# Kernel tuning notes

Measured on AMD Instinct MI355X. Metric: run time of the kernel, lower is better.

Reference implementation:

```python
import jax, jax.numpy as jnp
import numpy as np

D = 6
EPS = 1e-5


def layer_norm(x, w, b):
    m = jnp.mean(x, axis=-1, keepdims=True)
    v = jnp.mean(jnp.square(x - m), axis=-1, keepdims=True)
    return (x - m) * jax.lax.rsqrt(v + EPS) * w + b


def setup_inputs() -> dict:
    key = jax.random.key(0)
    ks = jax.random.split(key, 8)
    B, S = 8192, 128
    scale = 0.2
    return {
        "x": jax.random.normal(ks[0], (B, S, D), jnp.float32),
        "ln1_w": jnp.ones((D,), jnp.float32),
        "ln1_b": jnp.zeros((D,), jnp.float32),
        "wqkv": jax.random.normal(ks[1], (D, 3 * D), jnp.float32) * scale,
        "bqkv": jnp.zeros((3 * D,), jnp.float32),
        "wo": jax.random.normal(ks[2], (D, D), jnp.float32) * scale,
        "bo": jnp.zeros((D,), jnp.float32),
        "ln2_w": jnp.ones((D,), jnp.float32),
        "ln2_b": jnp.zeros((D,), jnp.float32),
        "w1": jax.random.normal(ks[3], (D, D), jnp.float32) * scale,
        "b1": jnp.zeros((D,), jnp.float32),
        "w2": jax.random.normal(ks[4], (D, D), jnp.float32) * scale,
        "b2": jnp.zeros((D,), jnp.float32),
    }


def reference(x, ln1_w, ln1_b, wqkv, bqkv, wo, bo, ln2_w, ln2_b, w1, b1, w2, b2):
    B, S, _ = x.shape
    # --- attention sub-block: x = x + attn(ln1(x)) ---
    h = layer_norm(x, ln1_w, ln1_b)                      # [B,S,D]
    qkv = h @ wqkv + bqkv                                # [B,S,3D]
    q, k, v = jnp.split(qkv, 3, axis=-1)
    scores = jnp.einsum('bqd,bkd->bqk', q, k) / jnp.sqrt(jnp.asarray(D, x.dtype))
    causal = jnp.tril(jnp.ones((S, S), bool))            # [S,S]
    scores = jnp.where(causal, scores, jnp.asarray(-1e9, x.dtype))
    attn = jax.nn.softmax(scores, axis=-1)               # [B,S,S]
    o = jnp.einsum('bqk,bkd->bqd', attn, v) @ wo + bo
    x = x + o
    # --- FFN sub-block: x = x + W2 @ gelu(W1 @ ln2(x)) ---
    h2 = layer_norm(x, ln2_w, ln2_b)
    ff = jax.nn.gelu(h2 @ w1 + b1, approximate=False) @ w2 + b2
    return x + ff
```

## Files before the change

kernel.cpp:

```cpp
#include <hip/hip_runtime.h>
#include <cmath>


typedef float    v2f  __attribute__((ext_vector_type(2)));
typedef float    f4v  __attribute__((ext_vector_type(4)));
typedef short    s4v  __attribute__((ext_vector_type(4)));
typedef uint32_t u2   __attribute__((ext_vector_type(2)));

constexpr int D = 6;
constexpr int S = 128;
#define EPS 1e-5f
#define RSQRT_D 0.4082482904638631f
#define LOG2E   1.4426950408889634f

#define EXP2F(x) __builtin_amdgcn_exp2f(x)
#define RCPF(x)  __builtin_amdgcn_rcpf(x)
#define PKFMA(a, b, c) __builtin_elementwise_fma((a), (b), (c))

union UA { uint32_t u[2]; u2 h; s4v v; };

__device__ __forceinline__ uint32_t pkbf(float hi, float lo) {
    return __builtin_amdgcn_perm(__builtin_bit_cast(uint32_t, hi),
                                 __builtin_bit_cast(uint32_t, lo),
                                 0x07060302u);
}
__device__ __forceinline__ uint16_t bf16t(float x) {
    return (uint16_t)(__builtin_bit_cast(uint32_t, x) >> 16);
}

__device__ __forceinline__ f4v mfma16(s4v a, s4v b, f4v c) {
#if __has_builtin(__builtin_amdgcn_mfma_f32_16x16x16bf16_1k)
    return __builtin_amdgcn_mfma_f32_16x16x16bf16_1k(a, b, c, 0, 0, 0);
#else
    f4v d;
    asm volatile("v_mfma_f32_16x16x16_bf16 %0, %1, %2, %3\n\t"
                 "s_nop 7\n\ts_nop 2"
                 : "=v"(d) : "v"(a), "v"(b), "v"(c));
    return d;
#endif
}

template<int QA, int QB>
__device__ __forceinline__ void attn_pair(
    const UA (&kf)[8], const UA (&vf)[8],
    UA qfA, UA qfB, float (*obuf)[10], int l15, int lq)
{
    const f4v z = {0.f, 0.f, 0.f, 0.f};
    f4v OA0 = z, OA1 = z, OB0 = z, OB1 = z;
    #pragma unroll
    for (int jt = 0; jt <= QB; ++jt) {
        f4v cB = mfma16(kf[jt].v, qfB.v, z);
        f4v cA;
        if (jt <= QA) cA = mfma16(kf[jt].v, qfA.v, z);
        float pB0 = EXP2F(cB[0]);
        float pB1 = EXP2F(cB[1]);
        float pB2 = EXP2F(cB[2]);
        float pB3 = EXP2F(cB[3]);
        if (jt == QB) {
            pB0 = (lq * 4 + 0 > l15) ? 0.f : pB0;
            pB1 = (lq * 4 + 1 > l15) ? 0.f : pB1;
            pB2 = (lq * 4 + 2 > l15) ? 0.f : pB2;
            pB3 = (lq * 4 + 3 > l15) ? 0.f : pB3;
        }
        UA paB;
        paB.u[0] = pkbf(pB1, pB0);
        paB.u[1] = pkbf(pB3, pB2);
        if (jt & 1) OB1 = mfma16(paB.v, vf[jt].v, OB1);
        else        OB0 = mfma16(paB.v, vf[jt].v, OB0);
        if (jt <= QA) {
            float pA0 = EXP2F(cA[0]);
            float pA1 = EXP2F(cA[1]);
            float pA2 = EXP2F(cA[2]);
            float pA3 = EXP2F(cA[3]);
            if (jt == QA) {
                pA0 = (lq * 4 + 0 > l15) ? 0.f : pA0;
                pA1 = (lq * 4 + 1 > l15) ? 0.f : pA1;
                pA2 = (lq * 4 + 2 > l15) ? 0.f : pA2;
                pA3 = (lq * 4 + 3 > l15) ? 0.f : pA3;
            }
            UA paA;
            paA.u[0] = pkbf(pA1, pA0);
            paA.u[1] = pkbf(pA3, pA2);
            if (jt & 1) OA1 = mfma16(paA.v, vf[jt].v, OA1);
            else        OA0 = mfma16(paA.v, vf[jt].v, OA0);
        }
    }
    f4v OA = OA0 + OA1;
    f4v OB = OB0 + OB1;
    if (l15 < 7) {
        #pragma unroll
        for (int r = 0; r < 4; ++r) {
            obuf[QA * 16 + lq * 4 + r][l15] = OA[r];
            obuf[QB * 16 + lq * 4 + r][l15] = OB[r];
        }
    }
}

__global__ __launch_bounds__(S, 4) void txblock_kernel(
    const float* __restrict__ x,
    const float* __restrict__ ln1_w, const float* __restrict__ ln1_b,
    const float* __restrict__ wqkv,  const float* __restrict__ bqkv,
    const float* __restrict__ wo,    const float* __restrict__ bo,
    const float* __restrict__ ln2_w, const float* __restrict__ ln2_b,
    const float* __restrict__ w1,    const float* __restrict__ b1,
    const float* __restrict__ w2,    const float* __restrict__ b2,
    float* __restrict__ out)
{
    __shared__ uint32_t qlds[S][6];
    __shared__ uint32_t klds[S][6];
    __shared__ uint16_t vt[8][S + 8];
    __shared__ float    obuf[S][10];

    const int b = blockIdx.x;
    const int s = threadIdx.x;
    const float* xrow = x + ((size_t)b * S + s) * D;
    float*      orow = out + ((size_t)b * S + s) * D;

    v2f xv01 = ((const v2f*)xrow)[0];
    v2f xv23 = ((const v2f*)xrow)[1];
    v2f xv45 = ((const v2f*)xrow)[2];
    float xv[D] = {xv01[0], xv01[1], xv23[0], xv23[1], xv45[0], xv45[1]};

    float m = 0.f;
    #pragma unroll
    for (int d = 0; d < D; ++d) m += xv[d];
    m *= (1.0f / D);
    float var = 0.f;
    #pragma unroll
    for (int d = 0; d < D; ++d) { float t = xv[d] - m; var += t * t; }
    var *= (1.0f / D);
    float rstd = rsqrtf(var + EPS);
    float h1[D];
    #pragma unroll
    for (int d = 0; d < D; ++d)
        h1[d] = (xv[d] - m) * rstd * ln1_w[d] + ln1_b[d];

    v2f aq[3], ak[3], av[3];
    #pragma unroll
    for (int jp = 0; jp < 3; ++jp) {
        aq[jp] = ((const v2f*)bqkv)[jp];
        ak[jp] = ((const v2f*)(bqkv + D))[jp];
        av[jp] = ((const v2f*)(bqkv + 2 * D))[jp];
    }
    #pragma unroll
    for (int d = 0; d < D; ++d) {
        const float* wrow = wqkv + d * 3 * D;
        v2f hd = {h1[d], h1[d]};
        #pragma unroll
        for (int jp = 0; jp < 3; ++jp) {
            aq[jp] = PKFMA(hd, ((const v2f*)wrow)[jp], aq[jp]);
            ak[jp] = PKFMA(hd, ((const v2f*)(wrow + D))[jp], ak[jp]);
            av[jp] = PKFMA(hd, ((const v2f*)(wrow + 2 * D))[jp], av[jp]);
        }
    }
    const v2f qscale = {RSQRT_D * LOG2E, RSQRT_D * LOG2E};

    #pragma unroll
    for (int jp = 0; jp < 3; ++jp) {
        v2f qs = aq[jp] * qscale;
        qlds[s][jp] = pkbf(qs[1], qs[0]);
        klds[s][jp] = pkbf(ak[jp][1], ak[jp][0]);
    }
    qlds[s][3] = 0; qlds[s][4] = 0; qlds[s][5] = 0;
    klds[s][3] = 0; klds[s][4] = 0; klds[s][5] = 0;
    vt[0][s] = bf16t(av[0][0]);
    vt[1][s] = bf16t(av[0][1]);
    vt[2][s] = bf16t(av[1][0]);
    vt[3][s] = bf16t(av[1][1]);
    vt[4][s] = bf16t(av[2][0]);
    vt[5][s] = bf16t(av[2][1]);
    vt[6][s] = 0x3F80;
    vt[7][s] = 0;
    __syncthreads();

    const int wv  = s >> 6;
    const int l15 = s & 15;
    const int lq  = (s >> 4) & 3;
    const int aoff = (lq < 2) ? lq * 8 : 16;
    const int vne  = (l15 < 7) ? l15 : 7;

    UA kf[8], vf[8];
    #pragma unroll
    for (int jt = 0; jt < 8; ++jt) {
        kf[jt].h = *(const u2*)((const char*)&klds[jt * 16 + l15][0] + aoff);
        vf[jt].h = *(const u2*)&vt[vne][jt * 16 + lq * 4];
    }

    if (wv == 0) {
        UA qA1, qB1, qA2, qB2;
        qA1.h = *(const u2*)((const char*)&qlds[0 * 16 + l15][0] + aoff);
        qB1.h = *(const u2*)((const char*)&qlds[7 * 16 + l15][0] + aoff);
        qA2.h = *(const u2*)((const char*)&qlds[3 * 16 + l15][0] + aoff);
        qB2.h = *(const u2*)((const char*)&qlds[4 * 16 + l15][0] + aoff);
        attn_pair<0, 7>(kf, vf, qA1, qB1, obuf, l15, lq);
        attn_pair<3, 4>(kf, vf, qA2, qB2, obuf, l15, lq);
    } else {
        UA qA1, qB1, qA2, qB2;
        qA1.h = *(const u2*)((const char*)&qlds[1 * 16 + l15][0] + aoff);
        qB1.h = *(const u2*)((const char*)&qlds[6 * 16 + l15][0] + aoff);
        qA2.h = *(const u2*)((const char*)&qlds[2 * 16 + l15][0] + aoff);
        qB2.h = *(const u2*)((const char*)&qlds[5 * 16 + l15][0] + aoff);
        attn_pair<1, 6>(kf, vf, qA1, qB1, obuf, l15, lq);
        attn_pair<2, 5>(kf, vf, qA2, qB2, obuf, l15, lq);
    }
    __syncthreads();

    v2f o01 = *(const v2f*)&obuf[s][0];
    v2f o23 = *(const v2f*)&obuf[s][2];
    v2f o45 = *(const v2f*)&obuf[s][4];
    float invl = RCPF(obuf[s][6]);
    v2f il = {invl, invl};
    o01 *= il; o23 *= il; o45 *= il;
    float av6[D] = {o01[0], o01[1], o23[0], o23[1], o45[0], o45[1]};

    v2f xvp[3] = {xv01, xv23, xv45};
    v2f x2p[3];
    #pragma unroll
    for (int dp = 0; dp < 3; ++dp) {
        v2f o = ((const v2f*)bo)[dp];
        #pragma unroll
        for (int e = 0; e < D; ++e) {
            v2f we = ((const v2f*)(wo + e * D))[dp];
            v2f ae = {av6[e], av6[e]};
            o = PKFMA(ae, we, o);
        }
        x2p[dp] = o + xvp[dp];
    }
    float x2[D] = {x2p[0][0], x2p[0][1], x2p[1][0], x2p[1][1], x2p[2][0], x2p[2][1]};

    float m2 = 0.f;
    #pragma unroll
    for (int d = 0; d < D; ++d) m2 += x2[d];
    m2 *= (1.0f / D);
    float var2 = 0.f;
    #pragma unroll
    for (int d = 0; d < D; ++d) { float t = x2[d] - m2; var2 += t * t; }
    var2 *= (1.0f / D);
    float rstd2 = rsqrtf(var2 + EPS);
    float h2[D];
    #pragma unroll
    for (int d = 0; d < D; ++d)
        h2[d] = (x2[d] - m2) * rstd2 * ln2_w[d] + ln2_b[d];

    v2f ap[3];
    #pragma unroll
    for (int jp = 0; jp < 3; ++jp) {
        v2f a = ((const v2f*)b1)[jp];
        #pragma unroll
        for (int d = 0; d < D; ++d) {
            v2f wd = ((const v2f*)(w1 + d * D))[jp];
            v2f hd = {h2[d], h2[d]};
            a = PKFMA(hd, wd, a);
        }
        ap[jp] = a;
    }
    float g[D];
    #pragma unroll
    for (int j = 0; j < D; ++j) {
        float a = ap[j >> 1][j & 1];
        float t  = a * a;
        float in = fmaf(0.044715f * t, a, a);
        float e  = EXP2F(in * -2.3022229f);
        float r  = RCPF(1.0f + e);
        g[j] = a * r;
    }
    #pragma unroll
    for (int dp = 0; dp < 3; ++dp) {
        v2f a = ((const v2f*)b2)[dp];
        #pragma unroll
        for (int e = 0; e < D; ++e) {
            v2f we = ((const v2f*)(w2 + e * D))[dp];
            v2f ge = {g[e], g[e]};
            a = PKFMA(ge, we, a);
        }
        ((v2f*)orow)[dp] = x2p[dp] + a;
    }
}

extern "C" void kernel_launch(void* const* d_in, const int* in_sizes, int n_in,
                              void* d_out, int out_size, void* d_ws, size_t ws_size,
                              hipStream_t stream) {
    const float* x     = (const float*)d_in[0];
    const float* ln1_w = (const float*)d_in[1];
    const float* ln1_b = (const float*)d_in[2];
    const float* wqkv  = (const float*)d_in[3];
    const float* bqkv  = (const float*)d_in[4];
    const float* wo    = (const float*)d_in[5];
    const float* bo    = (const float*)d_in[6];
    const float* ln2_w = (const float*)d_in[7];
    const float* ln2_b = (const float*)d_in[8];
    const float* w1    = (const float*)d_in[9];
    const float* b1    = (const float*)d_in[10];
    const float* w2    = (const float*)d_in[11];
    const float* b2    = (const float*)d_in[12];
    float* out = (float*)d_out;

    const int B = in_sizes[0] / (S * D);
    txblock_kernel<<<B, S, 0, stream>>>(x, ln1_w, ln1_b, wqkv, bqkv, wo, bo,
                                        ln2_w, ln2_b, w1, b1, w2, b2, out);
}
```

Before: 113.5 us.

## Process multiple batches per block with x prefetch and wave-local epilogue

Each block now loops over four batch elements, prefetching the next batch's input rows into registers while the current one is processed. The input row is stashed in shared memory so each wave can run the output projection and FFN on exactly the rows it produced in attention, removing the barrier between attention and epilogue. The split MFMA accumulators are merged into one chain. This reduces launch/block overhead and hides load latency, at the cost of fewer blocks and a longer dependent MFMA chain.

```diff
diff --git a/kernel.cpp b/kernel.cpp
--- a/kernel.cpp
+++ b/kernel.cpp
@@ -9,6 +9,7 @@
 
 constexpr int D = 6;
 constexpr int S = 128;
+constexpr int NB = 4;
 #define EPS 1e-5f
 #define RSQRT_D 0.4082482904638631f
 #define LOG2E   1.4426950408889634f
@@ -43,10 +44,10 @@
 template<int QA, int QB>
 __device__ __forceinline__ void attn_pair(
     const UA (&kf)[8], const UA (&vf)[8],
-    UA qfA, UA qfB, float (*obuf)[10], int l15, int lq)
+    UA qfA, UA qfB, float (*obuf)[14], int l15, int lq)
 {
     const f4v z = {0.f, 0.f, 0.f, 0.f};
-    f4v OA0 = z, OA1 = z, OB0 = z, OB1 = z;
+    f4v OA = z, OB = z;
     #pragma unroll
     for (int jt = 0; jt <= QB; ++jt) {
         f4v cB = mfma16(kf[jt].v, qfB.v, z);
@@ -65,8 +66,7 @@
         UA paB;
         paB.u[0] = pkbf(pB1, pB0);
         paB.u[1] = pkbf(pB3, pB2);
-        if (jt & 1) OB1 = mfma16(paB.v, vf[jt].v, OB1);
-        else        OB0 = mfma16(paB.v, vf[jt].v, OB0);
+        OB = mfma16(paB.v, vf[jt].v, OB);
         if (jt <= QA) {
             float pA0 = EXP2F(cA[0]);
             float pA1 = EXP2F(cA[1]);
@@ -81,12 +81,9 @@
             UA paA;
             paA.u[0] = pkbf(pA1, pA0);
             paA.u[1] = pkbf(pA3, pA2);
-            if (jt & 1) OA1 = mfma16(paA.v, vf[jt].v, OA1);
-            else        OA0 = mfma16(paA.v, vf[jt].v, OA0);
+            OA = mfma16(paA.v, vf[jt].v, OA);
         }
     }
-    f4v OA = OA0 + OA1;
-    f4v OB = OB0 + OB1;
     if (l15 < 7) {
         #pragma unroll
         for (int r = 0; r < 4; ++r) {
@@ -109,171 +106,191 @@
     __shared__ uint32_t qlds[S][6];
     __shared__ uint32_t klds[S][6];
     __shared__ uint16_t vt[8][S + 8];
-    __shared__ float    obuf[S][10];
-
-    const int b = blockIdx.x;
+    __shared__ float    obuf[S][14];
+
     const int s = threadIdx.x;
-    const float* xrow = x + ((size_t)b * S + s) * D;
-    float*      orow = out + ((size_t)b * S + s) * D;
-
-    v2f xv01 = ((const v2f*)xrow)[0];
-    v2f xv23 = ((const v2f*)xrow)[1];
-    v2f xv45 = ((const v2f*)xrow)[2];
-    float xv[D] = {xv01[0], xv01[1], xv23[0], xv23[1], xv45[0], xv45[1]};
-
-    float m = 0.f;
-    #pragma unroll
-    for (int d = 0; d < D; ++d) m += xv[d];
-    m *= (1.0f / D);
-    float var = 0.f;
-    #pragma unroll
-    for (int d = 0; d < D; ++d) { float t = xv[d] - m; var += t * t; }
-    var *= (1.0f / D);
-    float rstd = rsqrtf(var + EPS);
-    float h1[D];
-    #pragma unroll
-    for (int d = 0; d < D; ++d)
-        h1[d] = (xv[d] - m) * rstd * ln1_w[d] + ln1_b[d];
-
-    v2f aq[3], ak[3], av[3];
-    #pragma unroll
-    for (int jp = 0; jp < 3; ++jp) {
-        aq[jp] = ((const v2f*)bqkv)[jp];
-        ak[jp] = ((const v2f*)(bqkv + D))[jp];
-        av[jp] = ((const v2f*)(bqkv + 2 * D))[jp];
-    }
-    #pragma unroll
-    for (int d = 0; d < D; ++d) {
-        const float* wrow = wqkv + d * 3 * D;
-        v2f hd = {h1[d], h1[d]};
-        #pragma unroll
-        for (int jp = 0; jp < 3; ++jp) {
-            aq[jp] = PKFMA(hd, ((const v2f*)wrow)[jp], aq[jp]);
-            ak[jp] = PKFMA(hd, ((const v2f*)(wrow + D))[jp], ak[jp]);
-            av[jp] = PKFMA(hd, ((const v2f*)(wrow + 2 * D))[jp], av[jp]);
-        }
-    }
-    const v2f qscale = {RSQRT_D * LOG2E, RSQRT_D * LOG2E};
-
-    #pragma unroll
-    for (int jp = 0; jp < 3; ++jp) {
-        v2f qs = aq[jp] * qscale;
-        qlds[s][jp] = pkbf(qs[1], qs[0]);
-        klds[s][jp] = pkbf(ak[jp][1], ak[jp][0]);
-    }
-    qlds[s][3] = 0; qlds[s][4] = 0; qlds[s][5] = 0;
-    klds[s][3] = 0; klds[s][4] = 0; klds[s][5] = 0;
-    vt[0][s] = bf16t(av[0][0]);
-    vt[1][s] = bf16t(av[0][1]);
-    vt[2][s] = bf16t(av[1][0]);
-    vt[3][s] = bf16t(av[1][1]);
-    vt[4][s] = bf16t(av[2][0]);
-    vt[5][s] = bf16t(av[2][1]);
-    vt[6][s] = 0x3F80;
-    vt[7][s] = 0;
-    __syncthreads();
-
-    const int wv  = s >> 6;
+    const int t  = s & 63;
+    const int wv = s >> 6;
+    const int rrow = wv ? (t + 16 + ((t >= 32) ? 32 : 0))
+                        : (t + ((t >= 16) ? 32 : 0) + ((t >= 48) ? 32 : 0));
+
     const int l15 = s & 15;
     const int lq  = (s >> 4) & 3;
     const int aoff = (lq < 2) ? lq * 8 : 16;
     const int vne  = (l15 < 7) ? l15 : 7;
 
-    UA kf[8], vf[8];
-    #pragma unroll
-    for (int jt = 0; jt < 8; ++jt) {
-        kf[jt].h = *(const u2*)((const char*)&klds[jt * 16 + l15][0] + aoff);
-        vf[jt].h = *(const u2*)&vt[vne][jt * 16 + lq * 4];
-    }
-
-    if (wv == 0) {
-        UA qA1, qB1, qA2, qB2;
-        qA1.h = *(const u2*)((const char*)&qlds[0 * 16 + l15][0] + aoff);
-        qB1.h = *(const u2*)((const char*)&qlds[7 * 16 + l15][0] + aoff);
-        qA2.h = *(const u2*)((const char*)&qlds[3 * 16 + l15][0] + aoff);
-        qB2.h = *(const u2*)((const char*)&qlds[4 * 16 + l15][0] + aoff);
-        attn_pair<0, 7>(kf, vf, qA1, qB1, obuf, l15, lq);
-        attn_pair<3, 4>(kf, vf, qA2, qB2, obuf, l15, lq);
-    } else {
-        UA qA1, qB1, qA2, qB2;
-        qA1.h = *(const u2*)((const char*)&qlds[1 * 16 + l15][0] + aoff);
-        qB1.h = *(const u2*)((const char*)&qlds[6 * 16 + l15][0] + aoff);
-        qA2.h = *(const u2*)((const char*)&qlds[2 * 16 + l15][0] + aoff);
-        qB2.h = *(const u2*)((const char*)&qlds[5 * 16 + l15][0] + aoff);
-        attn_pair<1, 6>(kf, vf, qA1, qB1, obuf, l15, lq);
-        attn_pair<2, 5>(kf, vf, qA2, qB2, obuf, l15, lq);
-    }
-    __syncthreads();
-
-    v2f o01 = *(const v2f*)&obuf[s][0];
-    v2f o23 = *(const v2f*)&obuf[s][2];
-    v2f o45 = *(const v2f*)&obuf[s][4];
-    float invl = RCPF(obuf[s][6]);
-    v2f il = {invl, invl};
-    o01 *= il; o23 *= il; o45 *= il;
-    float av6[D] = {o01[0], o01[1], o23[0], o23[1], o45[0], o45[1]};
-
-    v2f xvp[3] = {xv01, xv23, xv45};
-    v2f x2p[3];
-    #pragma unroll
-    for (int dp = 0; dp < 3; ++dp) {
-        v2f o = ((const v2f*)bo)[dp];
-        #pragma unroll
-        for (int e = 0; e < D; ++e) {
-            v2f we = ((const v2f*)(wo + e * D))[dp];
-            v2f ae = {av6[e], av6[e]};
-            o = PKFMA(ae, we, o);
-        }
-        x2p[dp] = o + xvp[dp];
-    }
-    float x2[D] = {x2p[0][0], x2p[0][1], x2p[1][0], x2p[1][1], x2p[2][0], x2p[2][1]};
-
-    float m2 = 0.f;
-    #pragma unroll
-    for (int d = 0; d < D; ++d) m2 += x2[d];
-    m2 *= (1.0f / D);
-    float var2 = 0.f;
-    #pragma unroll
-    for (int d = 0; d < D; ++d) { float t = x2[d] - m2; var2 += t * t; }
-    var2 *= (1.0f / D);
-    float rstd2 = rsqrtf(var2 + EPS);
-    float h2[D];
-    #pragma unroll
-    for (int d = 0; d < D; ++d)
-        h2[d] = (x2[d] - m2) * rstd2 * ln2_w[d] + ln2_b[d];
-
-    v2f ap[3];
-    #pragma unroll
-    for (int jp = 0; jp < 3; ++jp) {
-        v2f a = ((const v2f*)b1)[jp];
+    size_t base = ((size_t)blockIdx.x * NB * S + s) * D;
+    const float* xrow = x + base;
+
+    v2f px01 = ((const v2f*)xrow)[0];
+    v2f px23 = ((const v2f*)xrow)[1];
+    v2f px45 = ((const v2f*)xrow)[2];
+
+    for (int it = 0; it < NB; ++it) {
+        const size_t bb = (size_t)blockIdx.x * NB + it;
+        float xv[D] = {px01[0], px01[1], px23[0], px23[1], px45[0], px45[1]};
+
+        float m = 0.f;
+        #pragma unroll
+        for (int d = 0; d < D; ++d) m += xv[d];
+        m *= (1.0f / D);
+        float var = 0.f;
+        #pragma unroll
+        for (int d = 0; d < D; ++d) { float tt = xv[d] - m; var += tt * tt; }
+        var *= (1.0f / D);
+        float rstd = rsqrtf(var + EPS);
+        float h1[D];
+        #pragma unroll
+        for (int d = 0; d < D; ++d)
+            h1[d] = (xv[d] - m) * rstd * ln1_w[d] + ln1_b[d];
+
+        v2f aq[3], ak[3], av[3];
+        #pragma unroll
+        for (int jp = 0; jp < 3; ++jp) {
+            aq[jp] = ((const v2f*)bqkv)[jp];
+            ak[jp] = ((const v2f*)(bqkv + D))[jp];
+            av[jp] = ((const v2f*)(bqkv + 2 * D))[jp];
+        }
         #pragma unroll
         for (int d = 0; d < D; ++d) {
-            v2f wd = ((const v2f*)(w1 + d * D))[jp];
-            v2f hd = {h2[d], h2[d]};
-            a = PKFMA(hd, wd, a);
-        }
-        ap[jp] = a;
-    }
-    float g[D];
-    #pragma unroll
-    for (int j = 0; j < D; ++j) {
-        float a = ap[j >> 1][j & 1];
-        float t  = a * a;
-        float in = fmaf(0.044715f * t, a, a);
-        float e  = EXP2F(in * -2.3022229f);
-        float r  = RCPF(1.0f + e);
-        g[j] = a * r;
-    }
-    #pragma unroll
-    for (int dp = 0; dp < 3; ++dp) {
-        v2f a = ((const v2f*)b2)[dp];
-        #pragma unroll
-        for (int e = 0; e < D; ++e) {
-            v2f we = ((const v2f*)(w2 + e * D))[dp];
-            v2f ge = {g[e], g[e]};
-            a = PKFMA(ge, we, a);
-        }
-        ((v2f*)orow)[dp] = x2p[dp] + a;
+            const float* wrow = wqkv + d * 3 * D;
+            v2f hd = {h1[d], h1[d]};
+            #pragma unroll
+            for (int jp = 0; jp < 3; ++jp) {
+                aq[jp] = PKFMA(hd, ((const v2f*)wrow)[jp], aq[jp]);
+                ak[jp] = PKFMA(hd, ((const v2f*)(wrow + D))[jp], ak[jp]);
+                av[jp] = PKFMA(hd, ((const v2f*)(wrow + 2 * D))[jp], av[jp]);
+            }
+        }
+        const v2f qscale = {RSQRT_D * LOG2E, RSQRT_D * LOG2E};
+
+        #pragma unroll
+        for (int jp = 0; jp < 3; ++jp) {
+            v2f qs = aq[jp] * qscale;
+            qlds[s][jp] = pkbf(qs[1], qs[0]);
+            klds[s][jp] = pkbf(ak[jp][1], ak[jp][0]);
+        }
+        qlds[s][3] = 0; qlds[s][4] = 0; qlds[s][5] = 0;
+        klds[s][3] = 0; klds[s][4] = 0; klds[s][5] = 0;
+        vt[0][s] = bf16t(av[0][0]);
+        vt[1][s] = bf16t(av[0][1]);
+        vt[2][s] = bf16t(av[1][0]);
+        vt[3][s] = bf16t(av[1][1]);
+        vt[4][s] = bf16t(av[2][0]);
+        vt[5][s] = bf16t(av[2][1]);
+        vt[6][s] = 0x3F80;
+        vt[7][s] = 0;
+        *(v2f*)&obuf[s][8]  = px01;
+        *(v2f*)&obuf[s][10] = px23;
+        *(v2f*)&obuf[s][12] = px45;
+
+        if (it + 1 < NB) {
+            const float* xn = xrow + (size_t)(it + 1) * S * D;
+            px01 = ((const v2f*)xn)[0];
+            px23 = ((const v2f*)xn)[1];
+            px45 = ((const v2f*)xn)[2];
+        }
+        __syncthreads();
+
+        UA kf[8], vf[8];
+        #pragma unroll
+        for (int jt = 0; jt < 8; ++jt) {
+            kf[jt].h = *(const u2*)((const char*)&klds[jt * 16 + l15][0] + aoff);
+            vf[jt].h = *(const u2*)&vt[vne][jt * 16 + lq * 4];
+        }
+        if (wv == 0) {
+            UA qA1, qB1, qA2, qB2;
+            qA1.h = *(const u2*)((const char*)&qlds[0 * 16 + l15][0] + aoff);
+            qB1.h = *(const u2*)((const char*)&qlds[7 * 16 + l15][0] + aoff);
+            qA2.h = *(const u2*)((const char*)&qlds[3 * 16 + l15][0] + aoff);
+            qB2.h = *(const u2*)((const char*)&qlds[4 * 16 + l15][0] + aoff);
+            attn_pair<0, 7>(kf, vf, qA1, qB1, obuf, l15, lq);
+            attn_pair<3, 4>(kf, vf, qA2, qB2, obuf, l15, lq);
+        } else {
+            UA qA1, qB1, qA2, qB2;
+            qA1.h = *(const u2*)((const char*)&qlds[1 * 16 + l15][0] + aoff);
+            qB1.h = *(const u2*)((const char*)&qlds[6 * 16 + l15][0] + aoff);
+            qA2.h = *(const u2*)((const char*)&qlds[2 * 16 + l15][0] + aoff);
+            qB2.h = *(const u2*)((const char*)&qlds[5 * 16 + l15][0] + aoff);
+            attn_pair<1, 6>(kf, vf, qA1, qB1, obuf, l15, lq);
+            attn_pair<2, 5>(kf, vf, qA2, qB2, obuf, l15, lq);
+        }
+
+        v2f rx01 = *(const v2f*)&obuf[rrow][8];
+        v2f rx23 = *(const v2f*)&obuf[rrow][10];
+        v2f rx45 = *(const v2f*)&obuf[rrow][12];
+        v2f o01 = *(const v2f*)&obuf[rrow][0];
+        v2f o23 = *(const v2f*)&obuf[rrow][2];
+        v2f o45 = *(const v2f*)&obuf[rrow][4];
+        float invl = RCPF(obuf[rrow][6]);
+        v2f il = {invl, invl};
+        o01 *= il; o23 *= il; o45 *= il;
+        float av6[D] = {o01[0], o01[1], o23[0], o23[1], o45[0], o45[1]};
+
+        v2f xvp[3] = {rx01, rx23, rx45};
+        v2f x2p[3];
+        #pragma unroll
+        for (int dp = 0; dp < 3; ++dp) {
+            v2f o = ((const v2f*)bo)[dp];
+            #pragma unroll
+            for (int e = 0; e < D; ++e) {
+                v2f we = ((const v2f*)(wo + e * D))[dp];
+                v2f ae = {av6[e], av6[e]};
+                o = PKFMA(ae, we, o);
+            }
+            x2p[dp] = o + xvp[dp];
+        }
+        float x2[D] = {x2p[0][0], x2p[0][1], x2p[1][0], x2p[1][1], x2p[2][0], x2p[2][1]};
+
+        float m2 = 0.f;
+        #pragma unroll
+        for (int d = 0; d < D; ++d) m2 += x2[d];
+        m2 *= (1.0f / D);
+        float var2 = 0.f;
+        #pragma unroll
+        for (int d = 0; d < D; ++d) { float tt = x2[d] - m2; var2 += tt * tt; }
+        var2 *= (1.0f / D);
+        float rstd2 = rsqrtf(var2 + EPS);
+        float h2[D];
+        #pragma unroll
+        for (int d = 0; d < D; ++d)
+            h2[d] = (x2[d] - m2) * rstd2 * ln2_w[d] + ln2_b[d];
+
+        v2f ap[3];
+        #pragma unroll
+        for (int jp = 0; jp < 3; ++jp) {
+            v2f a = ((const v2f*)b1)[jp];
+            #pragma unroll
+            for (int d = 0; d < D; ++d) {
+                v2f wd = ((const v2f*)(w1 + d * D))[jp];
+                v2f hd = {h2[d], h2[d]};
+                a = PKFMA(hd, wd, a);
+            }
+            ap[jp] = a;
+        }
+        float g[D];
+        #pragma unroll
+        for (int j = 0; j < D; ++j) {
+            float a = ap[j >> 1][j & 1];
+            float tt = a * a;
+            float in = fmaf(0.044715f * tt, a, a);
+            float e  = EXP2F(in * -2.3022229f);
+            float r  = RCPF(1.0f + e);
+            g[j] = a * r;
+        }
+        float* orow = out + (bb * S + rrow) * D;
+        #pragma unroll
+        for (int dp = 0; dp < 3; ++dp) {
+            v2f a = ((const v2f*)b2)[dp];
+            #pragma unroll
+            for (int e = 0; e < D; ++e) {
+                v2f we = ((const v2f*)(w2 + e * D))[dp];
+                v2f ge = {g[e], g[e]};
+                a = PKFMA(ge, we, a);
+            }
+            ((v2f*)orow)[dp] = x2p[dp] + a;
+        }
+        __syncthreads();
     }
 }
 
@@ -296,6 +313,7 @@
     float* out = (float*)d_out;
 
     const int B = in_sizes[0] / (S * D);
-    txblock_kernel<<<B, S, 0, stream>>>(x, ln1_w, ln1_b, wqkv, bqkv, wo, bo,
-                                        ln2_w, ln2_b, w1, b1, w2, b2, out);
-}
+    const int grid = B / NB;
+    txblock_kernel<<<grid, S, 0, stream>>>(x, ln1_w, ln1_b, wqkv, bqkv, wo, bo,
+                                           ln2_w, ln2_b, w1, b1, w2, b2, out);
+}
```

Measured after the change: 124.8 us. +9.9%, slower.
